# Optimization experiments

Hardware: AMD Instinct MI355X
Metric: run time of the kernel (lower is better)

## Reference

```python
import jax, jax.numpy as jnp
import numpy as np
import math

MAXL = 3
TAUS = [16, 16, 16, 16]
OUT_TAUS = [16, 16, 16, 16]
BM_CNT = 1.0
BM_EPS = 1e-5

# (l1, l2, l) triples in the kernel's triple-loop order, bucketed by output l
TRIPLES = {l: [] for l in range(MAXL + 1)}
for _l1 in range(MAXL + 1):
    for _l2 in range(_l1 + 1):
        for _l in range(_l1 - _l2, min(_l1 + _l2, MAXL) + 1):
            TRIPLES[_l].append((_l1, _l2))

MIDDLE_TAUS = [sum(TAUS[a] * TAUS[b] for (a, b) in TRIPLES[l]) for l in range(MAXL + 1)]


def _cg_coef(l1, m1, l2, m2, l, m):
    if m1 + m2 != m:
        return 0.0
    f = math.factorial
    pre = math.sqrt((2 * l + 1) * f(l1 + l2 - l) * f(l1 - l2 + l) * f(-l1 + l2 + l) / f(l1 + l2 + l + 1))
    pre *= math.sqrt(f(l + m) * f(l - m) * f(l1 - m1) * f(l1 + m1) * f(l2 - m2) * f(l2 + m2))
    s = 0.0
    for k in range(0, l1 + l2 - l + 1):
        d = [k, l1 + l2 - l - k, l1 - m1 - k, l2 + m2 - k, l - l2 + m1 + k, l - l1 - m2 + k]
        if any(x < 0 for x in d):
            continue
        den = 1.0
        for x in d:
            den *= f(x)
        s += (-1.0) ** k / den
    return pre * s


def _cg_tensor(l1, l2, l):
    t = np.zeros((2 * l1 + 1, 2 * l2 + 1, 2 * l + 1), dtype=np.float32)
    for i, m1 in enumerate(range(-l1, l1 + 1)):
        for j, m2 in enumerate(range(-l2, l2 + 1)):
            m = m1 + m2
            if -l <= m <= l:
                t[i, j, m + l] = _cg_coef(l1, m1, l2, m2, l, m)
    return t

CG = {}
for _l in range(MAXL + 1):
    for (_l1, _l2) in TRIPLES[_l]:
        CG[(_l1, _l2, _l)] = jnp.asarray(_cg_tensor(_l1, _l2, _l))

# complex-multiply contraction tensor: (a*b)[k] = a[i] b[j] CM[i,j,k]
_CM = np.zeros((2, 2, 2), dtype=np.float32)
_CM[0, 0, 0] = 1.0; _CM[1, 1, 0] = -1.0; _CM[0, 1, 1] = 1.0; _CM[1, 0, 1] = 1.0
CM = jnp.asarray(_CM)


def setup_inputs() -> dict:
    key = jax.random.key(0)
    k1, k2, k3 = jax.random.split(key, 3)
    in_len = sum(TAUS[l] * (2 * l + 1) for l in range(MAXL + 1))  # 256
    wlen = sum(OUT_TAUS[l] * MIDDLE_TAUS[l] for l in range(MAXL + 1))  # 90112
    activations = jax.random.normal(k1, (2048, in_len, 2), dtype=jnp.float32)
    W = 0.05 * jax.random.uniform(k2, (wlen, 2), dtype=jnp.float32)
    bn_stds = jax.random.uniform(k3, (sum(MIDDLE_TAUS),), dtype=jnp.float32)
    return {"activations": activations, "W": W, "bn_stds": bn_stds}


def reference(activations, W, bn_stds):
    B = activations.shape[0]
    # split input into per-l parts: [B, tau_l, 2l+1, 2]
    Fs = []
    st = 0
    for l in range(MAXL + 1):
        ln = TAUS[l] * (2 * l + 1)
        Fs.append(activations[:, st:st + ln, :].reshape(B, TAUS[l], 2 * l + 1, 2))
        st += ln
    outs = []
    w_st = 0
    s_st = 0
    for l in range(MAXL + 1):
        # Clebsch-Gordan products feeding output degree l
        mids = []
        for (l1, l2) in TRIPLES[l]:
            c = jnp.einsum('btmi,bsnj,mnp,ijk->btspk', Fs[l1], Fs[l2], CG[(l1, l2, l)], CM)
            mids.append(c.reshape(B, TAUS[l1] * TAUS[l2], 2 * l + 1, 2))
        mid = jnp.concatenate(mids, axis=1)  # [B, M_l, 2l+1, 2]
        Ml = MIDDLE_TAUS[l]
        # fused batchnorm: per-middle-channel std over batch and m, moving average update
        batch_std = jnp.sqrt(jnp.mean(jnp.sum(mid * mid, axis=-1), axis=(0, 2)))  # [M_l]
        mov = bn_stds[s_st:s_st + Ml]
        new_std = (mov * BM_CNT + batch_std) / (BM_CNT + 1.0)
        mid = mid / (new_std + BM_EPS)[None, :, None, None]
        # complex linear mix over middle channels -> out_taus[l]
        wl = jax.lax.dynamic_slice_in_dim(W, w_st, OUT_TAUS[l] * Ml, axis=0).reshape(OUT_TAUS[l], Ml, 2)
        out_l = jnp.einsum('oci,bcmj,ijk->bomk', wl, mid, CM)
        outs.append(out_l.reshape(B, OUT_TAUS[l] * (2 * l + 1), 2))
        w_st += OUT_TAUS[l] * Ml
        s_st += Ml
    return jnp.concatenate(outs, axis=1)  # [B, 256, 2]
```

## Files before the change

### kernel.cpp

```cpp
#include <hip/hip_runtime.h>
#include <math.h>

typedef __attribute__((ext_vector_type(8))) short bf16x8;
typedef __attribute__((ext_vector_type(4))) float f32x4;

constexpr double cfact(int n){ double r=1.0; for(int i=2;i<=n;++i) r*=(double)i; return r; }
constexpr double csqrt_(double x){ double g=(x>1.0)?x:1.0; for(int i=0;i<100;++i) g=0.5*(g+x/g); return g; }
constexpr double cg_coef_(int l1,int m1,int l2,int m2,int l,int m){
  double pre = csqrt_((double)(2*l+1)*cfact(l1+l2-l)*cfact(l1-l2+l)*cfact(-l1+l2+l)/cfact(l1+l2+l+1));
  pre = pre*csqrt_(cfact(l+m)*cfact(l-m)*cfact(l1-m1)*cfact(l1+m1)*cfact(l2-m2)*cfact(l2+m2));
  double s=0.0;
  for(int k=0;k<=l1+l2-l;++k){
    int d0=k,d1=l1+l2-l-k,d2=l1-m1-k,d3=l2+m2-k,d4=l-l2+m1+k,d5=l-l1-m2+k;
    if(d0<0||d1<0||d2<0||d3<0||d4<0||d5<0) continue;
    double den=cfact(d0)*cfact(d1)*cfact(d2)*cfact(d3)*cfact(d4)*cfact(d5);
    s+=((k&1)?-1.0:1.0)/den;
  }
  return pre*s;
}
struct CGList{ int n; float coef[64]; int mi[64]; int ni[64]; int pi[64]; };
constexpr CGList build_cg(int l1,int l2,int l){
  CGList T{};
  for(int i=0;i<2*l1+1;++i){
    for(int j=0;j<2*l2+1;++j){
      int m1=i-l1, m2=j-l2, m=m1+m2;
      if(m<-l||m>l) continue;
      double c=cg_coef_(l1,m1,l2,m2,l,m);
      if(c>1e-12||c<-1e-12){
        T.coef[T.n]=(float)c; T.mi[T.n]=i; T.ni[T.n]=j; T.pi[T.n]=m+l; T.n++;
      }
    }
  }
  return T;
}

__device__ __host__ constexpr int AOFF(int l){ return l==0?0: l==1?16: l==2?64:144; }
__device__ __host__ constexpr int MLs(int l){ return l==0?1024: l==1?1536: l==2?1792:1536; }
__device__ __host__ constexpr int WOFF(int l){ return l==0?0: l==1?16384: l==2?40960:69632; }
__device__ __host__ constexpr int SOFF(int l){ return l==0?0: l==1?1024: l==2?2560:4352; }
__device__ __host__ constexpr int ABASE(int l){ return l==0?0: l==1?65536: l==2?163840:278528; }

#define DEVFN __device__ __forceinline__
#define BP 68
#define AP 68


DEVFN unsigned f2bf2(float x, float y){
  unsigned ux = __float_as_uint(x); ux = (ux + 0x7FFFu + ((ux>>16)&1u)) >> 16;
  unsigned uy = __float_as_uint(y); uy = (uy + 0x7FFFu + ((uy>>16)&1u)) >> 16;
  return (ux & 0xFFFFu) | (uy << 16);
}

template<int L1,int L2,int L>
DEVFN void cg_accum(const float2* F1, const float2* F2, float2* mid){
  constexpr CGList T = build_cg(L1,L2,L);
  #pragma unroll
  for(int e=0;e<T.n;++e){
    const float c = T.coef[e];
    const float2 a = F1[T.mi[e]];
    const float2 b = F2[T.ni[e]];
    float pr = a.x*b.x - a.y*b.y;
    float pim= a.x*b.y + a.y*b.x;
    mid[T.pi[e]].x += c*pr;
    mid[T.pi[e]].y += c*pim;
  }
}

template<int L1,int L2,int L>
DEVFN void k1g(const float2* __restrict__ act2, int b0, int u, int bh,
               float& ssa, float& ssb){
  constexpr int N1=2*L1+1, N2=2*L2+1, NP=2*L+1;
  const int t = u>>3, s0 = (u&7)*2;
  const float2* base1  = act2 + AOFF(L1) + t*N1;
  const float2* base2a = act2 + AOFF(L2) + s0*N2;
  const float2* base2b = base2a + N2;
  #pragma unroll 2
  for(int bi=0;bi<16;++bi){
    const size_t ro = (size_t)(b0 + bh*16 + bi)*256;
    float2 F1[N1], F2a[N2], F2b[N2], mida[NP], midb[NP];
    #pragma unroll
    for(int m=0;m<N1;++m) F1[m]=base1[ro+m];
    #pragma unroll
    for(int n=0;n<N2;++n){ F2a[n]=base2a[ro+n]; F2b[n]=base2b[ro+n]; }
    #pragma unroll
    for(int p=0;p<NP;++p){ mida[p]=make_float2(0.f,0.f); midb[p]=make_float2(0.f,0.f); }
    cg_accum<L1,L2,L>(F1,F2a,mida);
    cg_accum<L1,L2,L>(F1,F2b,midb);
    #pragma unroll
    for(int p=0;p<NP;++p){
      ssa += mida[p].x*mida[p].x + mida[p].y*mida[p].y;
      ssb += midb[p].x*midb[p].x + midb[p].y*midb[p].y;
    }
  }
}

DEVFN void convW(const float* __restrict__ W, short* __restrict__ A, int idx){
  int l = (idx<1024)?0 : (idx<2560)?1 : (idx<4352)?2 : 3;
  int c = idx - SOFF(l);
  int Ml = MLs(l);
  const float2* wbase = (const float2*)W + WOFF(l) + c;
  unsigned* Aw = (unsigned*)(A + ABASE(l));
  #pragma unroll 4
  for(int o=0;o<16;++o){
    float2 w = wbase[(size_t)o*Ml];
    Aw[(size_t)o*Ml + c]      = f2bf2(w.x, -w.y);
    Aw[(size_t)(o+16)*Ml + c] = f2bf2(w.y,  w.x);
  }
}

__global__ __launch_bounds__(256) void k_sumsq(const float* __restrict__ act,
                                               float2* __restrict__ part,
                                               const float* __restrict__ W,
                                               short* __restrict__ A){
  const int bid = blockIdx.x;
  const int tid = threadIdx.x;
  if(bid >= 1472){
    convW(W, A, (bid-1472)*256 + tid);
    return;
  }
  const int order[23] = {22,16,21,18,15,20,13,9,14,8,17,7,12,6,10,3,5,19,2,11,1,4,0};
  const int ti = order[bid>>6];
  const int chunk = bid&63;
  const int b0 = chunk*32;
  const int u = tid & 127, bh = tid >> 7;
  const float2* act2 = (const float2*)act;
  float ssa=0.f, ssb=0.f;
  switch(ti){
    case 0:  k1g<0,0,0>(act2,b0,u,bh,ssa,ssb); break;
    case 1:  k1g<1,1,0>(act2,b0,u,bh,ssa,ssb); break;
    case 2:  k1g<2,2,0>(act2,b0,u,bh,ssa,ssb); break;
    case 3:  k1g<3,3,0>(act2,b0,u,bh,ssa,ssb); break;
    case 4:  k1g<1,0,1>(act2,b0,u,bh,ssa,ssb); break;
    case 5:  k1g<1,1,1>(act2,b0,u,bh,ssa,ssb); break;
    case 6:  k1g<2,1,1>(act2,b0,u,bh,ssa,ssb); break;
    case 7:  k1g<2,2,1>(act2,b0,u,bh,ssa,ssb); break;
    case 8:  k1g<3,2,1>(act2,b0,u,bh,ssa,ssb); break;
    case 9:  k1g<3,3,1>(act2,b0,u,bh,ssa,ssb); break;
    case 10: k1g<1,1,2>(act2,b0,u,bh,ssa,ssb); break;
    case 11: k1g<2,0,2>(act2,b0,u,bh,ssa,ssb); break;
    case 12: k1g<2,1,2>(act2,b0,u,bh,ssa,ssb); break;
    case 13: k1g<2,2,2>(act2,b0,u,bh,ssa,ssb); break;
    case 14: k1g<3,1,2>(act2,b0,u,bh,ssa,ssb); break;
    case 15: k1g<3,2,2>(act2,b0,u,bh,ssa,ssb); break;
    case 16: k1g<3,3,2>(act2,b0,u,bh,ssa,ssb); break;
    case 17: k1g<2,1,3>(act2,b0,u,bh,ssa,ssb); break;
    case 18: k1g<2,2,3>(act2,b0,u,bh,ssa,ssb); break;
    case 19: k1g<3,0,3>(act2,b0,u,bh,ssa,ssb); break;
    case 20: k1g<3,1,3>(act2,b0,u,bh,ssa,ssb); break;
    case 21: k1g<3,2,3>(act2,b0,u,bh,ssa,ssb); break;
    default: k1g<3,3,3>(act2,b0,u,bh,ssa,ssb); break;
  }
  part[(size_t)((ti*64 + chunk)*2 + bh)*128 + u] = make_float2(ssa, ssb);
}

__global__ __launch_bounds__(256) void k_scale(const float* __restrict__ bn,
                                               const float2* __restrict__ part,
                                               float* __restrict__ s){
  const int ti = blockIdx.x;
  const int ch = threadIdx.x;
  const int idx = ti*256 + ch;
  const int u = ch>>1;
  const float2* ps = part + (size_t)ti*128*128 + u;
  float sum = 0.f;
  #pragma unroll 8
  for(int r=0;r<128;++r){
    float2 v = ps[(size_t)r*128];
    sum += (ch&1) ? v.y : v.x;
  }
  int l = (idx<1024)?0 : (idx<2560)?1 : (idx<4352)?2 : 3;
  float divi = (l==0)?(1.f/2048.f) : (l==1)?(1.f/6144.f) : (l==2)?(1.f/10240.f) : (1.f/14336.f);
  float bstd = sqrtf(sum*divi);
  float nstd = 0.5f*(bn[idx]+bstd);
  s[idx] = 1.f/(nstd+1e-5f);
}


#define BT_B   0
#define LA_B   17408

template<int L1,int L2,int L,int Q,int NTIL>
DEVFN void kf_triple(const float2* __restrict__ act2, int b0, char* smem,
                     const unsigned* __restrict__ Aw,
                     const float* __restrict__ sg, f32x4& cR, f32x4& cI){
  constexpr int N1=2*L1+1, N2=2*L2+1, NP=2*L+1;
  constexpr int Ml = MLs(L);
  unsigned* btile  = (unsigned*)(smem + BT_B);
  unsigned* ldsA   = (unsigned*)(smem + LA_B);
  const int tid = threadIdx.x;
  const int lane = tid & 63, w = tid >> 6;
  const int col = lane & 15, quad = lane >> 4;
  const int up = tid & 31, bi = tid >> 5;
  const int r0 = tid>>4,       j0 = (tid&15)*4;
  const int r1 = (tid+256)>>4;
  const float2* arow = act2 + (size_t)(b0+bi)*256;
  uint4 v0 = *(const uint4*)(Aw + (size_t)r0*Ml + Q*256 + j0);
  uint4 v1 = *(const uint4*)(Aw + (size_t)r1*Ml + Q*256 + j0);
  #pragma unroll 1
  for(int cc=0; cc<4; ++cc){
    {
      const float2 s2 = *(const float2*)(sg + SOFF(L) + Q*256 + cc*64 + 2*up);
      const int u = cc*32 + up;
      const int t = u>>3, s0 = (u&7)*2;
      float2 F1[N1], F2a[N2], F2b[N2], mida[NP], midb[NP];
      #pragma unroll
      for(int m=0;m<N1;++m) F1[m]=arow[AOFF(L1)+t*N1+m];
      #pragma unroll
      for(int n=0;n<N2;++n){
        F2a[n]=arow[AOFF(L2)+s0*N2+n];
        F2b[n]=arow[AOFF(L2)+(s0+1)*N2+n];
      }
      #pragma unroll
      for(int p=0;p<NP;++p){ mida[p]=make_float2(0.f,0.f); midb[p]=make_float2(0.f,0.f); }
      cg_accum<L1,L2,L>(F1,F2a,mida);
      cg_accum<L1,L2,L>(F1,F2b,midb);
      #pragma unroll
      for(int p=0;p<NP;++p){
        uint2 v;
        v.x = f2bf2(mida[p].x*s2.x, mida[p].y*s2.x);
        v.y = f2bf2(midb[p].x*s2.y, midb[p].y*s2.y);
        *(uint2*)(btile + (size_t)(bi*NP+p)*BP + 2*up) = v;
      }
    }
    *(uint4*)(ldsA + r0*AP + j0) = v0;
    *(uint4*)(ldsA + r1*AP + j0) = v1;
    if(cc<3){
      const int base = Q*256 + (cc+1)*64;
      v0 = *(const uint4*)(Aw + (size_t)r0*Ml + base + j0);
      v1 = *(const uint4*)(Aw + (size_t)r1*Ml + base + j0);
    }
    __syncthreads();
    if(w < NTIL){
      const unsigned* ar0 = ldsA + col*AP + quad*4;
      const unsigned* ar1 = ldsA + (col+16)*AP + quad*4;
      const unsigned* bb  = btile + (w*16+col)*BP + quad*4;
      #pragma unroll
      for(int ks=0; ks<4; ++ks){
        bf16x8 b  = *(const bf16x8*)(bb + ks*16);
        bf16x8 A0 = *(const bf16x8*)(ar0 + ks*16);
        bf16x8 A1 = *(const bf16x8*)(ar1 + ks*16);
        cR = __builtin_amdgcn_mfma_f32_16x16x32_bf16(A0, b, cR, 0, 0, 0);
        cI = __builtin_amdgcn_mfma_f32_16x16x32_bf16(A1, b, cI, 0, 0, 0);
      }
    }
    __syncthreads();
  }
}

template<int L,int NTIL>
DEVFN void kf_epi(float* __restrict__ out, int b0, f32x4 cR, f32x4 cI){
  constexpr int NP = 2*L+1;
  const int tid = threadIdx.x, lane = tid & 63, w = tid >> 6;
  const int col = lane & 15, quad = lane >> 4;
  if(w < NTIL){
    const int r = w*16 + col;
    if(r < 8*NP){
      const int b = b0 + r/NP, p = r - (r/NP)*NP;
      float2* o2 = (float2*)out + (size_t)b*256 + AOFF(L);
      #pragma unroll
      for(int i=0;i<4;++i) o2[(quad*4+i)*NP + p] = make_float2(cR[i], cI[i]);
    }
  }
}

__global__ __launch_bounds__(256,3) void k_fusedall(const float* __restrict__ act,
    const short* __restrict__ A, const float* __restrict__ sg,
    float* __restrict__ out){
  __shared__ __align__(16) char smem[26112];
  const int bid = blockIdx.x;
  const float2* act2 = (const float2*)act;
  f32x4 cR={0.f,0.f,0.f,0.f}, cI={0.f,0.f,0.f,0.f};
  if(bid < 256){
    const int b0 = bid*8;
    const unsigned* Aw=(const unsigned*)(A+ABASE(3));
    kf_triple<2,1,3,0,4>(act2,b0,smem,Aw,sg,cR,cI);
    kf_triple<2,2,3,1,4>(act2,b0,smem,Aw,sg,cR,cI);
    kf_triple<3,0,3,2,4>(act2,b0,smem,Aw,sg,cR,cI);
    kf_triple<3,1,3,3,4>(act2,b0,smem,Aw,sg,cR,cI);
    kf_triple<3,2,3,4,4>(act2,b0,smem,Aw,sg,cR,cI);
    kf_triple<3,3,3,5,4>(act2,b0,smem,Aw,sg,cR,cI);
    kf_epi<3,4>(out,b0,cR,cI);
  } else if(bid < 512){
    const int b0 = (bid-256)*8;
    const unsigned* Aw=(const unsigned*)(A+ABASE(2));
    kf_triple<1,1,2,0,3>(act2,b0,smem,Aw,sg,cR,cI);
    kf_triple<2,0,2,1,3>(act2,b0,smem,Aw,sg,cR,cI);
    kf_triple<2,1,2,2,3>(act2,b0,smem,Aw,sg,cR,cI);
    kf_triple<2,2,2,3,3>(act2,b0,smem,Aw,sg,cR,cI);
    kf_triple<3,1,2,4,3>(act2,b0,smem,Aw,sg,cR,cI);
    kf_triple<3,2,2,5,3>(act2,b0,smem,Aw,sg,cR,cI);
    kf_triple<3,3,2,6,3>(act2,b0,smem,Aw,sg,cR,cI);
    kf_epi<2,3>(out,b0,cR,cI);
  } else if(bid < 768){
    const int b0 = (bid-512)*8;
    const unsigned* Aw=(const unsigned*)(A+ABASE(1));
    kf_triple<1,0,1,0,2>(act2,b0,smem,Aw,sg,cR,cI);
    kf_triple<1,1,1,1,2>(act2,b0,smem,Aw,sg,cR,cI);
    kf_triple<2,1,1,2,2>(act2,b0,smem,Aw,sg,cR,cI);
    kf_triple<2,2,1,3,2>(act2,b0,smem,Aw,sg,cR,cI);
    kf_triple<3,2,1,4,2>(act2,b0,smem,Aw,sg,cR,cI);
    kf_triple<3,3,1,5,2>(act2,b0,smem,Aw,sg,cR,cI);
    kf_epi<1,2>(out,b0,cR,cI);
  } else {
    const int b0 = (bid-768)*8;
    const unsigned* Aw=(const unsigned*)(A+ABASE(0));
    kf_triple<0,0,0,0,1>(act2,b0,smem,Aw,sg,cR,cI);
    kf_triple<1,1,0,1,1>(act2,b0,smem,Aw,sg,cR,cI);
    kf_triple<2,2,0,2,1>(act2,b0,smem,Aw,sg,cR,cI);
    kf_triple<3,3,0,3,1>(act2,b0,smem,Aw,sg,cR,cI);
    kf_epi<0,1>(out,b0,cR,cI);
  }
}

extern "C" void kernel_launch(void* const* d_in, const int* in_sizes, int n_in,
                              void* d_out, int out_size, void* d_ws, size_t ws_size,
                              hipStream_t stream) {
  const float* act = (const float*)d_in[0];
  const float* W   = (const float*)d_in[1];
  const float* bn  = (const float*)d_in[2];
  float* out = (float*)d_out;

  float*    s    = (float*)d_ws;
  short*    A    = (short*)((char*)d_ws + 24576);
  float2*   part = (float2*)((char*)d_ws + 1048576);

  hipLaunchKernelGGL(k_sumsq,   dim3(1495), dim3(256), 0, stream, act, part, W, A);
  hipLaunchKernelGGL(k_scale,   dim3(23),   dim3(256), 0, stream, bn, part, s);
  hipLaunchKernelGGL(k_fusedall,dim3(1024), dim3(256), 0, stream, act, A, s, out);
}
```

Measured before the change: 142.9 us.

## Exploit CG symmetry for diagonal l1==l2 triples in fused kernel

```diff
diff --git a/kernel.cpp b/kernel.cpp
--- a/kernel.cpp
+++ b/kernel.cpp
@@ -64,6 +64,18 @@
     mid[T.pi[e]].x += c*pr;
     mid[T.pi[e]].y += c*pim;
   }
+}
+
+DEVFN int diag_kpos(int t,int s){
+  if(t>s)  return 2*(t*(t-1)/2 + s);
+  if(t<s)  return 2*(s*(s-1)/2 + t) + 1;
+  return 240 + t;
+}
+DEVFN bool is_diag(int l,int q){
+  if(l==0) return true;
+  if(l==1) return q==1||q==3||q==5;
+  if(l==2) return q==0||q==3||q==6;
+  return q==1||q==5;
 }
 
 template<int L1,int L2,int L>
@@ -98,13 +110,18 @@
   int l = (idx<1024)?0 : (idx<2560)?1 : (idx<4352)?2 : 3;
   int c = idx - SOFF(l);
   int Ml = MLs(l);
+  int col = c;
+  {
+    int q = c>>8, cl = c&255;
+    if(is_diag(l,q)) col = q*256 + diag_kpos(cl>>4, cl&15);
+  }
   const float2* wbase = (const float2*)W + WOFF(l) + c;
   unsigned* Aw = (unsigned*)(A + ABASE(l));
   #pragma unroll 4
   for(int o=0;o<16;++o){
     float2 w = wbase[(size_t)o*Ml];
-    Aw[(size_t)o*Ml + c]      = f2bf2(w.x, -w.y);
-    Aw[(size_t)(o+16)*Ml + c] = f2bf2(w.y,  w.x);
+    Aw[(size_t)o*Ml + col]      = f2bf2(w.x, -w.y);
+    Aw[(size_t)(o+16)*Ml + col] = f2bf2(w.y,  w.x);
   }
 }
 
@@ -246,6 +263,105 @@
   }
 }
 
+template<int L1,int L,int Q,int NTIL>
+DEVFN void kf_tripleD(const float2* __restrict__ act2, int b0, char* smem,
+                      const unsigned* __restrict__ Aw,
+                      const float* __restrict__ sg, f32x4& cR, f32x4& cI){
+  constexpr int N1=2*L1+1, NP=2*L+1;
+  constexpr int Ml = MLs(L);
+  constexpr bool ODD = (L&1)!=0;
+  constexpr float SGN = ODD ? -1.f : 1.f;
+  unsigned* btile  = (unsigned*)(smem + BT_B);
+  unsigned* ldsA   = (unsigned*)(smem + LA_B);
+  const int tid = threadIdx.x;
+  const int lane = tid & 63, w = tid >> 6;
+  const int col = lane & 15, quad = lane >> 4;
+  const int up = tid & 31, bi = tid >> 5;
+  const int r0 = tid>>4,       j0 = (tid&15)*4;
+  const int r1 = (tid+256)>>4;
+  const float2* arow = act2 + (size_t)(b0+bi)*256;
+  const int sbase = SOFF(L) + Q*256;
+  uint4 v0 = *(const uint4*)(Aw + (size_t)r0*Ml + Q*256 + j0);
+  uint4 v1 = *(const uint4*)(Aw + (size_t)r1*Ml + Q*256 + j0);
+  #pragma unroll 1
+  for(int cc=0; cc<4; ++cc){
+    {
+      const int j = cc*32 + up;
+      if(j < 120){
+        int t = (int)(0.5f*(1.0f+sqrtf(8.f*(float)j+1.f)));
+        if(t*(t-1)/2 > j) t--;
+        else if(t*(t+1)/2 <= j) t++;
+        const int s = j - t*(t-1)/2;
+        const float sa = sg[sbase + t*16 + s];
+        const float sb = sg[sbase + s*16 + t];
+        float2 F1[N1], F2[N1], mid[NP];
+        #pragma unroll
+        for(int m=0;m<N1;++m){
+          F1[m]=arow[AOFF(L1)+t*N1+m];
+          F2[m]=arow[AOFF(L1)+s*N1+m];
+        }
+        #pragma unroll
+        for(int p=0;p<NP;++p) mid[p]=make_float2(0.f,0.f);
+        cg_accum<L1,L1,L>(F1,F2,mid);
+        #pragma unroll
+        for(int p=0;p<NP;++p){
+          uint2 v;
+          v.x = f2bf2(mid[p].x*sa, mid[p].y*sa);
+          v.y = f2bf2(SGN*mid[p].x*sb, SGN*mid[p].y*sb);
+          *(uint2*)(btile + (size_t)(bi*NP+p)*BP + 2*up) = v;
+        }
+      } else if(ODD){
+        #pragma unroll
+        for(int p=0;p<NP;++p)
+          *(uint2*)(btile + (size_t)(bi*NP+p)*BP + 2*up) = make_uint2(0u,0u);
+      } else {
+        const int d0 = 2*(j-120);
+        const float sa = sg[sbase + d0*17];
+        const float sb = sg[sbase + (d0+1)*17];
+        float2 Fa[N1], Fb[N1], mida[NP], midb[NP];
+        #pragma unroll
+        for(int m=0;m<N1;++m){
+          Fa[m]=arow[AOFF(L1)+d0*N1+m];
+          Fb[m]=arow[AOFF(L1)+(d0+1)*N1+m];
+        }
+        #pragma unroll
+        for(int p=0;p<NP;++p){ mida[p]=make_float2(0.f,0.f); midb[p]=make_float2(0.f,0.f); }
+        cg_accum<L1,L1,L>(Fa,Fa,mida);
+        cg_accum<L1,L1,L>(Fb,Fb,midb);
+        #pragma unroll
+        for(int p=0;p<NP;++p){
+          uint2 v;
+          v.x = f2bf2(mida[p].x*sa, mida[p].y*sa);
+          v.y = f2bf2(midb[p].x*sb, midb[p].y*sb);
+          *(uint2*)(btile + (size_t)(bi*NP+p)*BP + 2*up) = v;
+        }
+      }
+    }
+    *(uint4*)(ldsA + r0*AP + j0) = v0;
+    *(uint4*)(ldsA + r1*AP + j0) = v1;
+    if(cc<3){
+      const int base = Q*256 + (cc+1)*64;
+      v0 = *(const uint4*)(Aw + (size_t)r0*Ml + base + j0);
+      v1 = *(const uint4*)(Aw + (size_t)r1*Ml + base + j0);
+    }
+    __syncthreads();
+    if(w < NTIL){
+      const unsigned* ar0 = ldsA + col*AP + quad*4;
+      const unsigned* ar1 = ldsA + (col+16)*AP + quad*4;
+      const unsigned* bb  = btile + (w*16+col)*BP + quad*4;
+      #pragma unroll
+      for(int ks=0; ks<4; ++ks){
+        bf16x8 b  = *(const bf16x8*)(bb + ks*16);
+        bf16x8 A0 = *(const bf16x8*)(ar0 + ks*16);
+        bf16x8 A1 = *(const bf16x8*)(ar1 + ks*16);
+        cR = __builtin_amdgcn_mfma_f32_16x16x32_bf16(A0, b, cR, 0, 0, 0);
+        cI = __builtin_amdgcn_mfma_f32_16x16x32_bf16(A1, b, cI, 0, 0, 0);
+      }
+    }
+    __syncthreads();
+  }
+}
+
 template<int L,int NTIL>
 DEVFN void kf_epi(float* __restrict__ out, int b0, f32x4 cR, f32x4 cI){
   constexpr int NP = 2*L+1;
@@ -272,41 +388,41 @@
   if(bid < 256){
     const int b0 = bid*8;
     const unsigned* Aw=(const unsigned*)(A+ABASE(3));
-    kf_triple<2,1,3,0,4>(act2,b0,smem,Aw,sg,cR,cI);
-    kf_triple<2,2,3,1,4>(act2,b0,smem,Aw,sg,cR,cI);
-    kf_triple<3,0,3,2,4>(act2,b0,smem,Aw,sg,cR,cI);
-    kf_triple<3,1,3,3,4>(act2,b0,smem,Aw,sg,cR,cI);
-    kf_triple<3,2,3,4,4>(act2,b0,smem,Aw,sg,cR,cI);
-    kf_triple<3,3,3,5,4>(act2,b0,smem,Aw,sg,cR,cI);
+    kf_triple <2,1,3,0,4>(act2,b0,smem,Aw,sg,cR,cI);
+    kf_tripleD<2,  3,1,4>(act2,b0,smem,Aw,sg,cR,cI);
+    kf_triple <3,0,3,2,4>(act2,b0,smem,Aw,sg,cR,cI);
+    kf_triple <3,1,3,3,4>(act2,b0,smem,Aw,sg,cR,cI);
+    kf_triple <3,2,3,4,4>(act2,b0,smem,Aw,sg,cR,cI);
+    kf_tripleD<3,  3,5,4>(act2,b0,smem,Aw,sg,cR,cI);
     kf_epi<3,4>(out,b0,cR,cI);
   } else if(bid < 512){
     const int b0 = (bid-256)*8;
     const unsigned* Aw=(const unsigned*)(A+ABASE(2));
-    kf_triple<1,1,2,0,3>(act2,b0,smem,Aw,sg,cR,cI);
-    kf_triple<2,0,2,1,3>(act2,b0,smem,Aw,sg,cR,cI);
-    kf_triple<2,1,2,2,3>(act2,b0,smem,Aw,sg,cR,cI);
-    kf_triple<2,2,2,3,3>(act2,b0,smem,Aw,sg,cR,cI);
-    kf_triple<3,1,2,4,3>(act2,b0,smem,Aw,sg,cR,cI);
-    kf_triple<3,2,2,5,3>(act2,b0,smem,Aw,sg,cR,cI);
-    kf_triple<3,3,2,6,3>(act2,b0,smem,Aw,sg,cR,cI);
+    kf_tripleD<1,  2,0,3>(act2,b0,smem,Aw,sg,cR,cI);
+    kf_triple <2,0,2,1,3>(act2,b0,smem,Aw,sg,cR,cI);
+    kf_triple <2,1,2,2,3>(act2,b0,smem,Aw,sg,cR,cI);
+    kf_tripleD<2,  2,3,3>(act2,b0,smem,Aw,sg,cR,cI);
+    kf_triple <3,1,2,4,3>(act2,b0,smem,Aw,sg,cR,cI);
+    kf_triple <3,2,2,5,3>(act2,b0,smem,Aw,sg,cR,cI);
+    kf_tripleD<3,  2,6,3>(act2,b0,smem,Aw,sg,cR,cI);
     kf_epi<2,3>(out,b0,cR,cI);
   } else if(bid < 768){
     const int b0 = (bid-512)*8;
     const unsigned* Aw=(const unsigned*)(A+ABASE(1));
-    kf_triple<1,0,1,0,2>(act2,b0,smem,Aw,sg,cR,cI);
-    kf_triple<1,1,1,1,2>(act2,b0,smem,Aw,sg,cR,cI);
-    kf_triple<2,1,1,2,2>(act2,b0,smem,Aw,sg,cR,cI);
-    kf_triple<2,2,1,3,2>(act2,b0,smem,Aw,sg,cR,cI);
-    kf_triple<3,2,1,4,2>(act2,b0,smem,Aw,sg,cR,cI);
-    kf_triple<3,3,1,5,2>(act2,b0,smem,Aw,sg,cR,cI);
+    kf_triple <1,0,1,0,2>(act2,b0,smem,Aw,sg,cR,cI);
+    kf_tripleD<1,  1,1,2>(act2,b0,smem,Aw,sg,cR,cI);
+    kf_triple <2,1,1,2,2>(act2,b0,smem,Aw,sg,cR,cI);
+    kf_tripleD<2,  1,3,2>(act2,b0,smem,Aw,sg,cR,cI);
+    kf_triple <3,2,1,4,2>(act2,b0,smem,Aw,sg,cR,cI);
+    kf_tripleD<3,  1,5,2>(act2,b0,smem,Aw,sg,cR,cI);
     kf_epi<1,2>(out,b0,cR,cI);
   } else {
     const int b0 = (bid-768)*8;
     const unsigned* Aw=(const unsigned*)(A+ABASE(0));
-    kf_triple<0,0,0,0,1>(act2,b0,smem,Aw,sg,cR,cI);
-    kf_triple<1,1,0,1,1>(act2,b0,smem,Aw,sg,cR,cI);
-    kf_triple<2,2,0,2,1>(act2,b0,smem,Aw,sg,cR,cI);
-    kf_triple<3,3,0,3,1>(act2,b0,smem,Aw,sg,cR,cI);
+    kf_tripleD<0,  0,0,1>(act2,b0,smem,Aw,sg,cR,cI);
+    kf_tripleD<1,  0,1,1>(act2,b0,smem,Aw,sg,cR,cI);
+    kf_tripleD<2,  0,2,1>(act2,b0,smem,Aw,sg,cR,cI);
+    kf_tripleD<3,  0,3,1>(act2,b0,smem,Aw,sg,cR,cI);
     kf_epi<0,1>(out,b0,cR,cI);
   }
 }
```

Measured after the change: 145.9 us. 2.1% more time.
